# Kernel optimization log

Hardware: AMD Instinct MI355X
Metric: run time of the kernel (lower is better)

The kernel has to match this reference:

```python
import jax, jax.numpy as jnp
import numpy as np

B, V, E, L, D = 4, 64, 1024, 1024, 256  # batch, vertices, edges/graph, seq_len, d_model
DEG = E // V


def setup_inputs() -> dict:
    key = jax.random.key(0)
    k0, k1, k2, k3, k4, k5 = jax.random.split(key, 6)
    # fixed 16-regular graph, edges sorted by (src, dst) so that nonzero()
    # extraction order of the dense adjacency equals a gather at (src, dst)
    src = np.repeat(np.arange(V), DEG)
    dst = (src + 1 + np.tile(np.arange(DEG), V)) % V
    order = np.lexsort((dst, src))
    src, dst = src[order], dst[order]
    edge_index = jnp.asarray(np.stack([np.tile(src, B), np.tile(dst, B)]), dtype=jnp.int32)
    hidden_states = jax.random.normal(k0, (B * V, L, D), dtype=jnp.float32)
    edge_weight = jax.random.uniform(k1, (B * E,), dtype=jnp.float32, minval=0.1, maxval=1.0)
    s = 0.02
    Wq = jax.random.normal(k2, (D, D), dtype=jnp.float32) * s
    bq = jax.random.normal(k3, (D,), dtype=jnp.float32) * s
    Wk = jax.random.normal(k4, (D, D), dtype=jnp.float32) * s
    bk = jax.random.normal(k5, (D,), dtype=jnp.float32) * s
    attn_skip = jnp.float32(0.5)
    return {"hidden_states": hidden_states, "edge_index": edge_index, "edge_weight": edge_weight,
            "Wq": Wq, "bq": bq, "Wk": Wk, "bk": bk, "attn_skip": attn_skip}


def reference(hidden_states, edge_index, edge_weight, Wq, bq, Wk, bk, attn_skip):
    # broadcast static edge list / weights across time, as the torch repeat does
    ei = jnp.broadcast_to(edge_index[:, :, None], (2, B * E, L))
    ew = jnp.broadcast_to(edge_weight[:, None], (B * E, L))
    hs = hidden_states.reshape(B, V, L, D)
    Q = hs @ Wq.T + bq  # nn.Linear: x W^T + b
    K = hs @ Wk.T + bk
    att = jnp.einsum('bvld,bwld->bvwl', Q, K) / jnp.sqrt(jnp.float32(D))
    bidx = jnp.repeat(jnp.arange(B), E)
    src, dst = edge_index[0], edge_index[1]
    # to_dense_adj: scatter-add edge weights -> (B, V, V, L)
    adj = jnp.zeros((B, V, V, L), att.dtype).at[bidx, src, dst, :].add(ew)
    mask = jnp.where(adj > 0, 0.0, -jnp.inf)
    att = jax.nn.softmax(att + mask, axis=2)  # softmax over destination vertices w
    adj_new = attn_skip * adj + (1.0 - attn_skip) * att
    # dense_to_sparse: nonzeros in (graph=b*L+l, row, col) row-major order.
    # Edges are sorted by (src,dst), so this is a gather; torch flat order is (b, l, e):
    g = adj_new[bidx, src, dst, :]  # (B*E, L) ordered (b, e, l)
    flat = g.reshape(B, E, L).transpose(0, 2, 1).reshape(-1)  # order (b, l, e)
    # replicate the original .view(B, E, L).transpose(1, 2).reshape(B*E, L)
    ew_out = flat.reshape(B, E, L).transpose(0, 2, 1).reshape(B * E, L)
    return ei, ew_out
```

## Files before the change

### kernel.cpp

```cpp
#include <hip/hip_runtime.h>
#include <cstdint>
#include <cstddef>

constexpr int Bv = 4;
constexpr int Ev = 1024;
constexpr int Lv = 1024;
constexpr int BE = Bv * Ev;
constexpr size_t EI_PLANE = (size_t)BE * Lv;

constexpr int STRB = 264;

typedef __bf16 bf16x8 __attribute__((ext_vector_type(8)));
typedef __bf16 bf16x4 __attribute__((ext_vector_type(4)));
typedef __bf16 bf16x2 __attribute__((ext_vector_type(2)));
typedef float  f32x4  __attribute__((ext_vector_type(4)));

static __device__ __forceinline__ unsigned int pack_bf2(float lo, float hi) {
    union { bf16x2 h; unsigned int u; } c;
    c.h[0] = (__bf16)lo; c.h[1] = (__bf16)hi;
    return c.u;
}

__global__ __launch_bounds__(256) void precompute_kernel(
    const float* __restrict__ Wq, const float* __restrict__ Wk,
    const float* __restrict__ bq, __bf16* __restrict__ Mb, float* __restrict__ rv)
{
    const int blk = blockIdx.x;
    const int tid = threadIdx.x;
    if (blk < 256) {
        __shared__ float qs[256 * 17];
        __shared__ float ks[256 * 17];
        const int i16 = (blk >> 4) * 16;
        const int j16 = (blk & 15) * 16;
        const int c  = tid & 15;
        const int r0 = tid >> 4;
        #pragma unroll
        for (int it = 0; it < 16; ++it) {
            const int r = it * 16 + r0;
            qs[r * 17 + c] = Wq[r * 256 + i16 + c];
            ks[r * 17 + c] = Wk[r * 256 + j16 + c];
        }
        __syncthreads();
        const int dd = tid >> 4;
        const int tt = tid & 15;
        float a0 = 0.f, a1 = 0.f, a2 = 0.f, a3 = 0.f;
        for (int r = 0; r < 256; r += 4) {
            a0 = fmaf(qs[(r + 0) * 17 + dd], ks[(r + 0) * 17 + tt], a0);
            a1 = fmaf(qs[(r + 1) * 17 + dd], ks[(r + 1) * 17 + tt], a1);
            a2 = fmaf(qs[(r + 2) * 17 + dd], ks[(r + 2) * 17 + tt], a2);
            a3 = fmaf(qs[(r + 3) * 17 + dd], ks[(r + 3) * 17 + tt], a3);
        }
        const float m = ((a0 + a1) + (a2 + a3)) * 0.0625f;
        const int d = i16 + dd, t = j16 + tt;
        const int f    = (d >> 5) * 16 + (t >> 4);
        const int lane = ((d >> 3) & 3) * 16 + (t & 15);
        const int jj   = d & 7;
        Mb[((size_t)f * 64 + lane) * 8 + jj] = (__bf16)m;
    } else {
        __shared__ float bqs[256];
        bqs[tid] = bq[tid];
        __syncthreads();
        float a0 = 0.f, a1 = 0.f;
        for (int i = 0; i < 256; i += 2) {
            a0 = fmaf(bqs[i + 0], Wk[(i + 0) * 256 + tid], a0);
            a1 = fmaf(bqs[i + 1], Wk[(i + 1) * 256 + tid], a1);
        }
        rv[tid] = (a0 + a1) * 0.0625f;
    }
}

template <bool USE_WS>
__global__ __launch_bounds__(256) void edge_main(
    const float* __restrict__ hs, const int* __restrict__ eidx,
    const float* __restrict__ ew, const float* __restrict__ skipp,
    const __bf16* __restrict__ Mb, const float* __restrict__ rv,
    float* __restrict__ probs_or_out)
{
    __shared__ __bf16 hs_s[64 * STRB];
    float* S0 = (float*)hs_s;

    const int bl = blockIdx.x;
    const int b  = bl >> 10;
    const int l  = bl & 1023;
    const int tid  = threadIdx.x;
    const int w    = tid >> 6;
    const int lane = tid & 63;
    const int l15  = lane & 15;
    const int quad = lane >> 4;
    const int vgrp  = w >> 1;
    const int thalf = w & 1;

    {
        const float* base = hs + ((size_t)b * 64 * 1024 + (size_t)l) * 256;
        const int half = lane >> 5;
        const int c8   = (lane & 31) * 8;
        #pragma unroll
        for (int k = 0; k < 8; ++k) {
            const int v = k * 8 + w * 2 + half;
            const float* p = base + (size_t)v * (1024 * 256) + c8;
            float4 va = *(const float4*)p;
            float4 vb = *(const float4*)(p + 4);
            bf16x8 h;
            h[0] = (__bf16)va.x; h[1] = (__bf16)va.y;
            h[2] = (__bf16)va.z; h[3] = (__bf16)va.w;
            h[4] = (__bf16)vb.x; h[5] = (__bf16)vb.y;
            h[6] = (__bf16)vb.z; h[7] = (__bf16)vb.w;
            *(bf16x8*)(&hs_s[v * STRB + c8]) = h;
        }
    }
    __syncthreads();

    f32x4 s_acc[2][2];
    #pragma unroll
    for (int mi = 0; mi < 2; ++mi)
        #pragma unroll
        for (int sl = 0; sl < 2; ++sl) {
            s_acc[mi][sl][0] = 0.f; s_acc[mi][sl][1] = 0.f;
            s_acc[mi][sl][2] = 0.f; s_acc[mi][sl][3] = 0.f;
        }

    const int vt0 = vgrp * 2;

    #pragma unroll 1
    for (int pp = 0; pp < 4; ++pp) {
        const int p = thalf * 4 + pp;
        f32x4 acc[2][2];
        #pragma unroll
        for (int tt = 0; tt < 2; ++tt) {
            const f32x4 rb = *(const f32x4*)(rv + (2 * p + tt) * 16 + quad * 4);
            acc[tt][0] = rb;
            acc[tt][1] = rb;
        }
        #pragma unroll
        for (int kt = 0; kt < 8; ++kt) {
            const bf16x8 mfr0 = *(const bf16x8*)(Mb +
                ((size_t)((kt * 16 + 2 * p + 0) * 64 + lane)) * 8);
            const bf16x8 mfr1 = *(const bf16x8*)(Mb +
                ((size_t)((kt * 16 + 2 * p + 1) * 64 + lane)) * 8);
            #pragma unroll
            for (int mi = 0; mi < 2; ++mi) {
                const bf16x8 hfr = *(const bf16x8*)(
                    &hs_s[((vt0 + mi) * 16 + l15) * STRB + kt * 32 + quad * 8]);
                acc[0][mi] = __builtin_amdgcn_mfma_f32_16x16x32_bf16(
                    mfr0, hfr, acc[0][mi], 0, 0, 0);
                acc[1][mi] = __builtin_amdgcn_mfma_f32_16x16x32_bf16(
                    mfr1, hfr, acc[1][mi], 0, 0, 0);
            }
        }
        #pragma unroll
        for (int mi = 0; mi < 2; ++mi) {
            const int m = vt0 + mi;
            unsigned int Ar = pack_bf2(acc[0][mi][0], acc[0][mi][1]);
            unsigned int Br = pack_bf2(acc[0][mi][2], acc[0][mi][3]);
            unsigned int Cr = pack_bf2(acc[1][mi][0], acc[1][mi][1]);
            unsigned int Dr = pack_bf2(acc[1][mi][2], acc[1][mi][3]);
            asm("v_permlane32_swap_b32 %0, %1" : "+v"(Ar), "+v"(Cr));
            asm("v_permlane16_swap_b32 %0, %1" : "+v"(Ar), "+v"(Cr));
            asm("v_permlane32_swap_b32 %0, %1" : "+v"(Br), "+v"(Dr));
            asm("v_permlane16_swap_b32 %0, %1" : "+v"(Br), "+v"(Dr));
            union { uint4 u; bf16x8 h; } fr;
            fr.u = make_uint4(Ar, Br, Cr, Dr);
            const bf16x8 brow0 = *(const bf16x8*)(
                &hs_s[(m * 16 + l15) * STRB + p * 32 + quad * 8]);
            const bf16x8 brow1 = *(const bf16x8*)(
                &hs_s[(((m + 1) & 3) * 16 + l15) * STRB + p * 32 + quad * 8]);
            s_acc[mi][0] = __builtin_amdgcn_mfma_f32_16x16x32_bf16(
                fr.h, brow0, s_acc[mi][0], 0, 0, 0);
            s_acc[mi][1] = __builtin_amdgcn_mfma_f32_16x16x32_bf16(
                fr.h, brow1, s_acc[mi][1], 0, 0, 0);
        }
    }
    __syncthreads();

    if (!thalf) {
        #pragma unroll
        for (int mi = 0; mi < 2; ++mi)
            #pragma unroll
            for (int sl = 0; sl < 2; ++sl)
                #pragma unroll
                for (int r = 0; r < 4; ++r)
                    S0[((vt0 + mi) * 16 + quad * 4 + r) * 36 + sl * 16 + l15] =
                        s_acc[mi][sl][r];
    }
    __syncthreads();
    if (thalf) {
        #pragma unroll
        for (int mi = 0; mi < 2; ++mi)
            #pragma unroll
            for (int sl = 0; sl < 2; ++sl)
                #pragma unroll
                for (int r = 0; r < 4; ++r)
                    S0[((vt0 + mi) * 16 + quad * 4 + r) * 36 + sl * 16 + l15] +=
                        s_acc[mi][sl][r];
    }
    __syncthreads();

    const int e0  = tid * 4;
    const int be0 = b * Ev + e0;
    int srcs[4], dsts[4];
    #pragma unroll
    for (int j = 0; j < 4; ++j) {
        srcs[j] = eidx[be0 + j];
        dsts[j] = eidx[BE + be0 + j];
    }
    float lg[4];
    #pragma unroll
    for (int j = 0; j < 4; ++j) {
        const int slot = ((dsts[j] >> 4) - (srcs[j] >> 4)) & 3;
        lg[j] = S0[srcs[j] * 36 + slot * 16 + (dsts[j] & 15)];
    }

    float mx = fmaxf(fmaxf(lg[0], lg[1]), fmaxf(lg[2], lg[3]));
    mx = fmaxf(mx, __shfl_xor(mx, 1));
    mx = fmaxf(mx, __shfl_xor(mx, 2));
    float ex[4], sm = 0.f;
    #pragma unroll
    for (int j = 0; j < 4; ++j) { ex[j] = __expf(lg[j] - mx); sm += ex[j]; }
    sm += __shfl_xor(sm, 1);
    sm += __shfl_xor(sm, 2);
    const float inv = 1.0f / sm;

    if (USE_WS) {
        float4 o = make_float4(ex[0] * inv, ex[1] * inv, ex[2] * inv, ex[3] * inv);
        *(float4*)(probs_or_out + (size_t)bl * 1024 + e0) = o;
    } else {
        const float skip = skipp[0];
        const float om = 1.0f - skip;
        #pragma unroll
        for (int j = 0; j < 4; ++j) {
            float g = fmaf(skip, ew[be0 + j], om * (ex[j] * inv));
            probs_or_out[(size_t)(be0 + j) * Lv + l] = g;
        }
    }
}

__global__ __launch_bounds__(256) void output_kernel(
    const float* __restrict__ probs, const int* __restrict__ eidx,
    const float* __restrict__ ew, const float* __restrict__ skipp,
    float* __restrict__ out)
{
    __shared__ float tile[64 * 68];
    const int lt = blockIdx.x;
    const int et = blockIdx.y;
    const int b  = blockIdx.z;
    const int t  = threadIdx.x;
    const int tr = t >> 4;
    const int tc = t & 15;

    #pragma unroll
    for (int q = 0; q < 4; ++q) {
        const int lloc = q * 16 + tr;
        float4 v = *(const float4*)(probs +
            ((size_t)(b * 1024 + lt * 64 + lloc)) * 1024 + et * 64 + tc * 4);
        *(float4*)(&tile[lloc * 68 + tc * 4]) = v;
    }
    __syncthreads();

    const float skip = skipp[0];
    const float om = 1.0f - skip;
    float* out_ei0 = out;
    float* out_ei1 = out + EI_PLANE;
    float* out_ew  = out + 2 * EI_PLANE;

    #pragma unroll
    for (int q = 0; q < 4; ++q) {
        const int eloc = q * 16 + tr;
        const int be = b * Ev + et * 64 + eloc;
        const float w  = ew[be];
        const float sv = (float)eidx[be];
        const float dv = (float)eidx[BE + be];
        const int lloc0 = tc * 4;
        float4 o;
        o.x = fmaf(skip, w, om * tile[(lloc0 + 0) * 68 + eloc]);
        o.y = fmaf(skip, w, om * tile[(lloc0 + 1) * 68 + eloc]);
        o.z = fmaf(skip, w, om * tile[(lloc0 + 2) * 68 + eloc]);
        o.w = fmaf(skip, w, om * tile[(lloc0 + 3) * 68 + eloc]);
        const size_t off = (size_t)be * Lv + lt * 64 + lloc0;
        *(float4*)(out_ew  + off) = o;
        *(float4*)(out_ei0 + off) = make_float4(sv, sv, sv, sv);
        *(float4*)(out_ei1 + off) = make_float4(dv, dv, dv, dv);
    }
}

__global__ __launch_bounds__(256) void ei_kernel(
    const int* __restrict__ eidx, float* __restrict__ out)
{
    const int blk = blockIdx.x;
    const int c = blk >> 12;
    const int j = blk & 4095;
    const float v = (float)eidx[c * BE + j];
    float4 o = make_float4(v, v, v, v);
    *(float4*)(out + (size_t)blk * 1024 + threadIdx.x * 4) = o;
}

extern "C" void kernel_launch(void* const* d_in, const int* in_sizes, int n_in,
                              void* d_out, int out_size, void* d_ws, size_t ws_size,
                              hipStream_t stream)
{
    const float* hs   = (const float*)d_in[0];
    const int*   eidx = (const int*)d_in[1];
    const float* ew   = (const float*)d_in[2];
    const float* Wq   = (const float*)d_in[3];
    const float* bq   = (const float*)d_in[4];
    const float* Wk   = (const float*)d_in[5];
    const float* skip = (const float*)d_in[7];

    char* wsb = (char*)d_ws;
    __bf16* Mb   = (__bf16*)wsb;
    float*  rv   = (float*)(wsb + 131072);
    float*  probs = (float*)(wsb + 132096);
    const size_t need = 132096 + (size_t)Bv * Lv * Ev * sizeof(float);

    precompute_kernel<<<dim3(257), dim3(256), 0, stream>>>(Wq, Wk, bq, Mb, rv);

    if (ws_size >= need) {
        edge_main<true><<<dim3(Bv * Lv), dim3(256), 0, stream>>>(
            hs, eidx, ew, skip, Mb, rv, probs);
        output_kernel<<<dim3(16, 16, 4), dim3(256), 0, stream>>>(
            probs, eidx, ew, skip, (float*)d_out);
    } else {
        float* out_ew = (float*)d_out + 2 * EI_PLANE;
        edge_main<false><<<dim3(Bv * Lv), dim3(256), 0, stream>>>(
            hs, eidx, ew, skip, Mb, rv, out_ew);
        ei_kernel<<<dim3(2 * BE), dim3(256), 0, stream>>>(eidx, (float*)d_out);
    }
}
```

Measured before the change: 445.0 us.

## Process eight time steps per block with double-buffered register prefetch of hidden states

```diff
diff --git a/kernel.cpp b/kernel.cpp
--- a/kernel.cpp
+++ b/kernel.cpp
@@ -9,6 +9,7 @@
 constexpr size_t EI_PLANE = (size_t)BE * Lv;
 
 constexpr int STRB = 264;
+constexpr int NL = 8;
 
 typedef __bf16 bf16x8 __attribute__((ext_vector_type(8)));
 typedef __bf16 bf16x4 __attribute__((ext_vector_type(4)));
@@ -70,18 +71,17 @@
 }
 
 template <bool USE_WS>
-__global__ __launch_bounds__(256) void edge_main(
+__global__ __launch_bounds__(256, 2) void edge_main(
     const float* __restrict__ hs, const int* __restrict__ eidx,
     const float* __restrict__ ew, const float* __restrict__ skipp,
     const __bf16* __restrict__ Mb, const float* __restrict__ rv,
     float* __restrict__ probs_or_out)
 {
-    __shared__ __bf16 hs_s[64 * STRB];
-    float* S0 = (float*)hs_s;
-
-    const int bl = blockIdx.x;
-    const int b  = bl >> 10;
-    const int l  = bl & 1023;
+    __shared__ __bf16 hs2_s[2][64 * STRB];
+
+    const int blk = blockIdx.x;
+    const int b   = blk >> 7;
+    const int l0  = (blk & 127) * NL;
     const int tid  = threadIdx.x;
     const int w    = tid >> 6;
     const int lane = tid & 63;
@@ -89,11 +89,25 @@
     const int quad = lane >> 4;
     const int vgrp  = w >> 1;
     const int thalf = w & 1;
+    const int vt0   = vgrp * 2;
+    const int half  = lane >> 5;
+    const int c8    = (lane & 31) * 8;
+
+    const float* hb = hs + (size_t)b * 65536 * 256;
+
+    const int e0  = tid * 4;
+    const int be0 = b * Ev + e0;
+    int soff[4];
+    #pragma unroll
+    for (int j = 0; j < 4; ++j) {
+        const int src = eidx[be0 + j];
+        const int dst = eidx[BE + be0 + j];
+        const int slot = ((dst >> 4) - (src >> 4)) & 3;
+        soff[j] = src * 36 + slot * 16 + (dst & 15);
+    }
 
     {
-        const float* base = hs + ((size_t)b * 64 * 1024 + (size_t)l) * 256;
-        const int half = lane >> 5;
-        const int c8   = (lane & 31) * 8;
+        const float* base = hb + (size_t)l0 * 256;
         #pragma unroll
         for (int k = 0; k < 8; ++k) {
             const int v = k * 8 + w * 2 + half;
@@ -105,132 +119,154 @@
             h[2] = (__bf16)va.z; h[3] = (__bf16)va.w;
             h[4] = (__bf16)vb.x; h[5] = (__bf16)vb.y;
             h[6] = (__bf16)vb.z; h[7] = (__bf16)vb.w;
-            *(bf16x8*)(&hs_s[v * STRB + c8]) = h;
+            *(bf16x8*)(&hs2_s[0][v * STRB + c8]) = h;
         }
     }
     __syncthreads();
 
-    f32x4 s_acc[2][2];
-    #pragma unroll
-    for (int mi = 0; mi < 2; ++mi)
-        #pragma unroll
-        for (int sl = 0; sl < 2; ++sl) {
-            s_acc[mi][sl][0] = 0.f; s_acc[mi][sl][1] = 0.f;
-            s_acc[mi][sl][2] = 0.f; s_acc[mi][sl][3] = 0.f;
-        }
-
-    const int vt0 = vgrp * 2;
-
+    int cur = 0;
     #pragma unroll 1
-    for (int pp = 0; pp < 4; ++pp) {
-        const int p = thalf * 4 + pp;
-        f32x4 acc[2][2];
-        #pragma unroll
-        for (int tt = 0; tt < 2; ++tt) {
-            const f32x4 rb = *(const f32x4*)(rv + (2 * p + tt) * 16 + quad * 4);
-            acc[tt][0] = rb;
-            acc[tt][1] = rb;
-        }
-        #pragma unroll
-        for (int kt = 0; kt < 8; ++kt) {
-            const bf16x8 mfr0 = *(const bf16x8*)(Mb +
-                ((size_t)((kt * 16 + 2 * p + 0) * 64 + lane)) * 8);
-            const bf16x8 mfr1 = *(const bf16x8*)(Mb +
-                ((size_t)((kt * 16 + 2 * p + 1) * 64 + lane)) * 8);
+    for (int i = 0; i < NL; ++i) {
+        const int l = l0 + i;
+        __bf16* bufc = &hs2_s[cur][0];
+        float*  S0   = (float*)bufc;
+
+        const int lnext = (i + 1 < NL) ? (l + 1) : l;
+        const float* basen = hb + (size_t)lnext * 256;
+        float4 pf[16];
+        #pragma unroll
+        for (int k = 0; k < 8; ++k) {
+            const float* p = basen + (size_t)(k * 8 + w * 2 + half) * (1024 * 256) + c8;
+            pf[2 * k]     = *(const float4*)p;
+            pf[2 * k + 1] = *(const float4*)(p + 4);
+        }
+
+        f32x4 s_acc[2][2];
+        #pragma unroll
+        for (int mi = 0; mi < 2; ++mi)
+            #pragma unroll
+            for (int sl = 0; sl < 2; ++sl) {
+                s_acc[mi][sl][0] = 0.f; s_acc[mi][sl][1] = 0.f;
+                s_acc[mi][sl][2] = 0.f; s_acc[mi][sl][3] = 0.f;
+            }
+
+        #pragma unroll 1
+        for (int pp = 0; pp < 4; ++pp) {
+            const int p = thalf * 4 + pp;
+            f32x4 acc[2][2];
+            #pragma unroll
+            for (int tt = 0; tt < 2; ++tt) {
+                const f32x4 rb = *(const f32x4*)(rv + (2 * p + tt) * 16 + quad * 4);
+                acc[tt][0] = rb;
+                acc[tt][1] = rb;
+            }
+            #pragma unroll
+            for (int kt = 0; kt < 8; ++kt) {
+                const bf16x8 mfr0 = *(const bf16x8*)(Mb +
+                    ((size_t)((kt * 16 + 2 * p + 0) * 64 + lane)) * 8);
+                const bf16x8 mfr1 = *(const bf16x8*)(Mb +
+                    ((size_t)((kt * 16 + 2 * p + 1) * 64 + lane)) * 8);
+                #pragma unroll
+                for (int mi = 0; mi < 2; ++mi) {
+                    const bf16x8 hfr = *(const bf16x8*)(
+                        &bufc[((vt0 + mi) * 16 + l15) * STRB + kt * 32 + quad * 8]);
+                    acc[0][mi] = __builtin_amdgcn_mfma_f32_16x16x32_bf16(
+                        mfr0, hfr, acc[0][mi], 0, 0, 0);
+                    acc[1][mi] = __builtin_amdgcn_mfma_f32_16x16x32_bf16(
+                        mfr1, hfr, acc[1][mi], 0, 0, 0);
+                }
+            }
             #pragma unroll
             for (int mi = 0; mi < 2; ++mi) {
-                const bf16x8 hfr = *(const bf16x8*)(
-                    &hs_s[((vt0 + mi) * 16 + l15) * STRB + kt * 32 + quad * 8]);
-                acc[0][mi] = __builtin_amdgcn_mfma_f32_16x16x32_bf16(
-                    mfr0, hfr, acc[0][mi], 0, 0, 0);
-                acc[1][mi] = __builtin_amdgcn_mfma_f32_16x16x32_bf16(
-                    mfr1, hfr, acc[1][mi], 0, 0, 0);
-            }
-        }
-        #pragma unroll
-        for (int mi = 0; mi < 2; ++mi) {
-            const int m = vt0 + mi;
-            unsigned int Ar = pack_bf2(acc[0][mi][0], acc[0][mi][1]);
-            unsigned int Br = pack_bf2(acc[0][mi][2], acc[0][mi][3]);
-            unsigned int Cr = pack_bf2(acc[1][mi][0], acc[1][mi][1]);
-            unsigned int Dr = pack_bf2(acc[1][mi][2], acc[1][mi][3]);
-            asm("v_permlane32_swap_b32 %0, %1" : "+v"(Ar), "+v"(Cr));
-            asm("v_permlane16_swap_b32 %0, %1" : "+v"(Ar), "+v"(Cr));
-            asm("v_permlane32_swap_b32 %0, %1" : "+v"(Br), "+v"(Dr));
-            asm("v_permlane16_swap_b32 %0, %1" : "+v"(Br), "+v"(Dr));
-            union { uint4 u; bf16x8 h; } fr;
-            fr.u = make_uint4(Ar, Br, Cr, Dr);
-            const bf16x8 brow0 = *(const bf16x8*)(
-                &hs_s[(m * 16 + l15) * STRB + p * 32 + quad * 8]);
-            const bf16x8 brow1 = *(const bf16x8*)(
-                &hs_s[(((m + 1) & 3) * 16 + l15) * STRB + p * 32 + quad * 8]);
-            s_acc[mi][0] = __builtin_amdgcn_mfma_f32_16x16x32_bf16(
-                fr.h, brow0, s_acc[mi][0], 0, 0, 0);
-            s_acc[mi][1] = __builtin_amdgcn_mfma_f32_16x16x32_bf16(
-                fr.h, brow1, s_acc[mi][1], 0, 0, 0);
-        }
-    }
-    __syncthreads();
-
-    if (!thalf) {
-        #pragma unroll
-        for (int mi = 0; mi < 2; ++mi)
-            #pragma unroll
-            for (int sl = 0; sl < 2; ++sl)
+                const int m = vt0 + mi;
+                unsigned int Ar = pack_bf2(acc[0][mi][0], acc[0][mi][1]);
+                unsigned int Br = pack_bf2(acc[0][mi][2], acc[0][mi][3]);
+                unsigned int Cr = pack_bf2(acc[1][mi][0], acc[1][mi][1]);
+                unsigned int Dr = pack_bf2(acc[1][mi][2], acc[1][mi][3]);
+                asm("v_permlane32_swap_b32 %0, %1" : "+v"(Ar), "+v"(Cr));
+                asm("v_permlane16_swap_b32 %0, %1" : "+v"(Ar), "+v"(Cr));
+                asm("v_permlane32_swap_b32 %0, %1" : "+v"(Br), "+v"(Dr));
+                asm("v_permlane16_swap_b32 %0, %1" : "+v"(Br), "+v"(Dr));
+                union { uint4 u; bf16x8 h; } fr;
+                fr.u = make_uint4(Ar, Br, Cr, Dr);
+                const bf16x8 brow0 = *(const bf16x8*)(
+                    &bufc[(m * 16 + l15) * STRB + p * 32 + quad * 8]);
+                const bf16x8 brow1 = *(const bf16x8*)(
+                    &bufc[(((m + 1) & 3) * 16 + l15) * STRB + p * 32 + quad * 8]);
+                s_acc[mi][0] = __builtin_amdgcn_mfma_f32_16x16x32_bf16(
+                    fr.h, brow0, s_acc[mi][0], 0, 0, 0);
+                s_acc[mi][1] = __builtin_amdgcn_mfma_f32_16x16x32_bf16(
+                    fr.h, brow1, s_acc[mi][1], 0, 0, 0);
+            }
+        }
+        __syncthreads();
+
+        if (!thalf) {
+            #pragma unroll
+            for (int mi = 0; mi < 2; ++mi)
                 #pragma unroll
-                for (int r = 0; r < 4; ++r)
-                    S0[((vt0 + mi) * 16 + quad * 4 + r) * 36 + sl * 16 + l15] =
-                        s_acc[mi][sl][r];
-    }
-    __syncthreads();
-    if (thalf) {
-        #pragma unroll
-        for (int mi = 0; mi < 2; ++mi)
-            #pragma unroll
-            for (int sl = 0; sl < 2; ++sl)
+                for (int sl = 0; sl < 2; ++sl)
+                    #pragma unroll
+                    for (int r = 0; r < 4; ++r)
+                        S0[((vt0 + mi) * 16 + quad * 4 + r) * 36 + sl * 16 + l15] =
+                            s_acc[mi][sl][r];
+        }
+        __syncthreads();
+        if (thalf) {
+            #pragma unroll
+            for (int mi = 0; mi < 2; ++mi)
                 #pragma unroll
-                for (int r = 0; r < 4; ++r)
-                    S0[((vt0 + mi) * 16 + quad * 4 + r) * 36 + sl * 16 + l15] +=
-                        s_acc[mi][sl][r];
-    }
-    __syncthreads();
-
-    const int e0  = tid * 4;
-    const int be0 = b * Ev + e0;
-    int srcs[4], dsts[4];
-    #pragma unroll
-    for (int j = 0; j < 4; ++j) {
-        srcs[j] = eidx[be0 + j];
-        dsts[j] = eidx[BE + be0 + j];
-    }
-    float lg[4];
-    #pragma unroll
-    for (int j = 0; j < 4; ++j) {
-        const int slot = ((dsts[j] >> 4) - (srcs[j] >> 4)) & 3;
-        lg[j] = S0[srcs[j] * 36 + slot * 16 + (dsts[j] & 15)];
-    }
-
-    float mx = fmaxf(fmaxf(lg[0], lg[1]), fmaxf(lg[2], lg[3]));
-    mx = fmaxf(mx, __shfl_xor(mx, 1));
-    mx = fmaxf(mx, __shfl_xor(mx, 2));
-    float ex[4], sm = 0.f;
-    #pragma unroll
-    for (int j = 0; j < 4; ++j) { ex[j] = __expf(lg[j] - mx); sm += ex[j]; }
-    sm += __shfl_xor(sm, 1);
-    sm += __shfl_xor(sm, 2);
-    const float inv = 1.0f / sm;
-
-    if (USE_WS) {
-        float4 o = make_float4(ex[0] * inv, ex[1] * inv, ex[2] * inv, ex[3] * inv);
-        *(float4*)(probs_or_out + (size_t)bl * 1024 + e0) = o;
-    } else {
-        const float skip = skipp[0];
-        const float om = 1.0f - skip;
-        #pragma unroll
-        for (int j = 0; j < 4; ++j) {
-            float g = fmaf(skip, ew[be0 + j], om * (ex[j] * inv));
-            probs_or_out[(size_t)(be0 + j) * Lv + l] = g;
-        }
+                for (int sl = 0; sl < 2; ++sl)
+                    #pragma unroll
+                    for (int r = 0; r < 4; ++r)
+                        S0[((vt0 + mi) * 16 + quad * 4 + r) * 36 + sl * 16 + l15] +=
+                            s_acc[mi][sl][r];
+        }
+        __syncthreads();
+
+        float lg[4];
+        #pragma unroll
+        for (int j = 0; j < 4; ++j)
+            lg[j] = S0[soff[j]];
+
+        float mx = fmaxf(fmaxf(lg[0], lg[1]), fmaxf(lg[2], lg[3]));
+        mx = fmaxf(mx, __shfl_xor(mx, 1));
+        mx = fmaxf(mx, __shfl_xor(mx, 2));
+        float ex[4], sm = 0.f;
+        #pragma unroll
+        for (int j = 0; j < 4; ++j) { ex[j] = __expf(lg[j] - mx); sm += ex[j]; }
+        sm += __shfl_xor(sm, 1);
+        sm += __shfl_xor(sm, 2);
+        const float inv = 1.0f / sm;
+
+        if (USE_WS) {
+            float4 o = make_float4(ex[0] * inv, ex[1] * inv, ex[2] * inv, ex[3] * inv);
+            *(float4*)(probs_or_out + ((size_t)(b * 1024 + l)) * 1024 + e0) = o;
+        } else {
+            const float skip = skipp[0];
+            const float om = 1.0f - skip;
+            #pragma unroll
+            for (int j = 0; j < 4; ++j) {
+                float g = fmaf(skip, ew[be0 + j], om * (ex[j] * inv));
+                probs_or_out[(size_t)(be0 + j) * Lv + l] = g;
+            }
+        }
+
+        {
+            __bf16* bufn = &hs2_s[cur ^ 1][0];
+            #pragma unroll
+            for (int k = 0; k < 8; ++k) {
+                const int v = k * 8 + w * 2 + half;
+                bf16x8 h;
+                h[0] = (__bf16)pf[2 * k].x;     h[1] = (__bf16)pf[2 * k].y;
+                h[2] = (__bf16)pf[2 * k].z;     h[3] = (__bf16)pf[2 * k].w;
+                h[4] = (__bf16)pf[2 * k + 1].x; h[5] = (__bf16)pf[2 * k + 1].y;
+                h[6] = (__bf16)pf[2 * k + 1].z; h[7] = (__bf16)pf[2 * k + 1].w;
+                *(bf16x8*)(&bufn[v * STRB + c8]) = h;
+            }
+        }
+        __syncthreads();
+        cur ^= 1;
     }
 }
 
@@ -314,13 +350,13 @@
     precompute_kernel<<<dim3(257), dim3(256), 0, stream>>>(Wq, Wk, bq, Mb, rv);
 
     if (ws_size >= need) {
-        edge_main<true><<<dim3(Bv * Lv), dim3(256), 0, stream>>>(
+        edge_main<true><<<dim3(Bv * Lv / NL), dim3(256), 0, stream>>>(
             hs, eidx, ew, skip, Mb, rv, probs);
         output_kernel<<<dim3(16, 16, 4), dim3(256), 0, stream>>>(
             probs, eidx, ew, skip, (float*)d_out);
     } else {
         float* out_ew = (float*)d_out + 2 * EI_PLANE;
-        edge_main<false><<<dim3(Bv * Lv), dim3(256), 0, stream>>>(
+        edge_main<false><<<dim3(Bv * Lv / NL), dim3(256), 0, stream>>>(
             hs, eidx, ew, skip, Mb, rv, out_ew);
         ei_kernel<<<dim3(2 * BE), dim3(256), 0, stream>>>(eidx, (float*)d_out);
     }
```

Measured after the change: 476.9 us. +7.2%, slower.

## Give each wave one vertex tile across all p-chunks, dropping split-K reduction

Applied to the files above, without the earlier changes.

```diff
diff --git a/kernel.cpp b/kernel.cpp
--- a/kernel.cpp
+++ b/kernel.cpp
@@ -70,7 +70,7 @@
 }
 
 template <bool USE_WS>
-__global__ __launch_bounds__(256) void edge_main(
+__global__ __launch_bounds__(256, 4) void edge_main(
     const float* __restrict__ hs, const int* __restrict__ eidx,
     const float* __restrict__ ew, const float* __restrict__ skipp,
     const __bf16* __restrict__ Mb, const float* __restrict__ rv,
@@ -87,8 +87,18 @@
     const int lane = tid & 63;
     const int l15  = lane & 15;
     const int quad = lane >> 4;
-    const int vgrp  = w >> 1;
-    const int thalf = w & 1;
+    const int nt1  = (w + 1) & 3;
+
+    const int e0  = tid * 4;
+    const int be0 = b * Ev + e0;
+    int soff[4];
+    #pragma unroll
+    for (int j = 0; j < 4; ++j) {
+        const int src = eidx[be0 + j];
+        const int dst = eidx[BE + be0 + j];
+        const int slot = ((dst >> 4) - (src >> 4)) & 3;
+        soff[j] = src * 36 + slot * 16 + (dst & 15);
+    }
 
     {
         const float* base = hs + ((size_t)b * 64 * 1024 + (size_t)l) * 256;
@@ -110,105 +120,70 @@
     }
     __syncthreads();
 
-    f32x4 s_acc[2][2];
-    #pragma unroll
-    for (int mi = 0; mi < 2; ++mi)
+    bf16x8 hfrK[8];
+    #pragma unroll
+    for (int kt = 0; kt < 8; ++kt)
+        hfrK[kt] = *(const bf16x8*)(&hs_s[(w * 16 + l15) * STRB + kt * 32 + quad * 8]);
+
+    f32x4 s_acc0, s_acc1;
+    s_acc0[0] = 0.f; s_acc0[1] = 0.f; s_acc0[2] = 0.f; s_acc0[3] = 0.f;
+    s_acc1 = s_acc0;
+
+    #pragma unroll 1
+    for (int p = 0; p < 8; ++p) {
+        f32x4 acc0 = *(const f32x4*)(rv + (2 * p + 0) * 16 + quad * 4);
+        f32x4 acc1 = *(const f32x4*)(rv + (2 * p + 1) * 16 + quad * 4);
         #pragma unroll
-        for (int sl = 0; sl < 2; ++sl) {
-            s_acc[mi][sl][0] = 0.f; s_acc[mi][sl][1] = 0.f;
-            s_acc[mi][sl][2] = 0.f; s_acc[mi][sl][3] = 0.f;
-        }
-
-    const int vt0 = vgrp * 2;
-
-    #pragma unroll 1
-    for (int pp = 0; pp < 4; ++pp) {
-        const int p = thalf * 4 + pp;
-        f32x4 acc[2][2];
-        #pragma unroll
-        for (int tt = 0; tt < 2; ++tt) {
-            const f32x4 rb = *(const f32x4*)(rv + (2 * p + tt) * 16 + quad * 4);
-            acc[tt][0] = rb;
-            acc[tt][1] = rb;
-        }
-        #pragma unroll
-        for (int kt = 0; kt < 8; ++kt) {
-            const bf16x8 mfr0 = *(const bf16x8*)(Mb +
-                ((size_t)((kt * 16 + 2 * p + 0) * 64 + lane)) * 8);
-            const bf16x8 mfr1 = *(const bf16x8*)(Mb +
-                ((size_t)((kt * 16 + 2 * p + 1) * 64 + lane)) * 8);
+        for (int kh = 0; kh < 2; ++kh) {
+            bf16x8 m0[4], m1[4];
             #pragma unroll
-            for (int mi = 0; mi < 2; ++mi) {
-                const bf16x8 hfr = *(const bf16x8*)(
-                    &hs_s[((vt0 + mi) * 16 + l15) * STRB + kt * 32 + quad * 8]);
-                acc[0][mi] = __builtin_amdgcn_mfma_f32_16x16x32_bf16(
-                    mfr0, hfr, acc[0][mi], 0, 0, 0);
-                acc[1][mi] = __builtin_amdgcn_mfma_f32_16x16x32_bf16(
-                    mfr1, hfr, acc[1][mi], 0, 0, 0);
+            for (int k2 = 0; k2 < 4; ++k2) {
+                const int kt = kh * 4 + k2;
+                m0[k2] = *(const bf16x8*)(Mb +
+                    ((size_t)((kt * 16 + 2 * p + 0) * 64 + lane)) * 8);
+                m1[k2] = *(const bf16x8*)(Mb +
+                    ((size_t)((kt * 16 + 2 * p + 1) * 64 + lane)) * 8);
             }
-        }
-        #pragma unroll
-        for (int mi = 0; mi < 2; ++mi) {
-            const int m = vt0 + mi;
-            unsigned int Ar = pack_bf2(acc[0][mi][0], acc[0][mi][1]);
-            unsigned int Br = pack_bf2(acc[0][mi][2], acc[0][mi][3]);
-            unsigned int Cr = pack_bf2(acc[1][mi][0], acc[1][mi][1]);
-            unsigned int Dr = pack_bf2(acc[1][mi][2], acc[1][mi][3]);
-            asm("v_permlane32_swap_b32 %0, %1" : "+v"(Ar), "+v"(Cr));
-            asm("v_permlane16_swap_b32 %0, %1" : "+v"(Ar), "+v"(Cr));
-            asm("v_permlane32_swap_b32 %0, %1" : "+v"(Br), "+v"(Dr));
-            asm("v_permlane16_swap_b32 %0, %1" : "+v"(Br), "+v"(Dr));
-            union { uint4 u; bf16x8 h; } fr;
-            fr.u = make_uint4(Ar, Br, Cr, Dr);
-            const bf16x8 brow0 = *(const bf16x8*)(
-                &hs_s[(m * 16 + l15) * STRB + p * 32 + quad * 8]);
-            const bf16x8 brow1 = *(const bf16x8*)(
-                &hs_s[(((m + 1) & 3) * 16 + l15) * STRB + p * 32 + quad * 8]);
-            s_acc[mi][0] = __builtin_amdgcn_mfma_f32_16x16x32_bf16(
-                fr.h, brow0, s_acc[mi][0], 0, 0, 0);
-            s_acc[mi][1] = __builtin_amdgcn_mfma_f32_16x16x32_bf16(
-                fr.h, brow1, s_acc[mi][1], 0, 0, 0);
-        }
+            #pragma unroll
+            for (int k2 = 0; k2 < 4; ++k2) {
+                const int kt = kh * 4 + k2;
+                acc0 = __builtin_amdgcn_mfma_f32_16x16x32_bf16(
+                    m0[k2], hfrK[kt], acc0, 0, 0, 0);
+                acc1 = __builtin_amdgcn_mfma_f32_16x16x32_bf16(
+                    m1[k2], hfrK[kt], acc1, 0, 0, 0);
+            }
+        }
+        unsigned int Ar = pack_bf2(acc0[0], acc0[1]);
+        unsigned int Br = pack_bf2(acc0[2], acc0[3]);
+        unsigned int Cr = pack_bf2(acc1[0], acc1[1]);
+        unsigned int Dr = pack_bf2(acc1[2], acc1[3]);
+        asm("v_permlane32_swap_b32 %0, %1" : "+v"(Ar), "+v"(Cr));
+        asm("v_permlane16_swap_b32 %0, %1" : "+v"(Ar), "+v"(Cr));
+        asm("v_permlane32_swap_b32 %0, %1" : "+v"(Br), "+v"(Dr));
+        asm("v_permlane16_swap_b32 %0, %1" : "+v"(Br), "+v"(Dr));
+        union { uint4 u; bf16x8 h; } fr;
+        fr.u = make_uint4(Ar, Br, Cr, Dr);
+
+        const bf16x8 brow0 = *(const bf16x8*)(
+            &hs_s[(w * 16 + l15) * STRB + p * 32 + quad * 8]);
+        const bf16x8 brow1 = *(const bf16x8*)(
+            &hs_s[(nt1 * 16 + l15) * STRB + p * 32 + quad * 8]);
+        s_acc0 = __builtin_amdgcn_mfma_f32_16x16x32_bf16(fr.h, brow0, s_acc0, 0, 0, 0);
+        s_acc1 = __builtin_amdgcn_mfma_f32_16x16x32_bf16(fr.h, brow1, s_acc1, 0, 0, 0);
     }
     __syncthreads();
 
-    if (!thalf) {
-        #pragma unroll
-        for (int mi = 0; mi < 2; ++mi)
-            #pragma unroll
-            for (int sl = 0; sl < 2; ++sl)
-                #pragma unroll
-                for (int r = 0; r < 4; ++r)
-                    S0[((vt0 + mi) * 16 + quad * 4 + r) * 36 + sl * 16 + l15] =
-                        s_acc[mi][sl][r];
+    #pragma unroll
+    for (int r = 0; r < 4; ++r) {
+        S0[(w * 16 + quad * 4 + r) * 36 +  0 + l15] = s_acc0[r];
+        S0[(w * 16 + quad * 4 + r) * 36 + 16 + l15] = s_acc1[r];
     }
     __syncthreads();
-    if (thalf) {
-        #pragma unroll
-        for (int mi = 0; mi < 2; ++mi)
-            #pragma unroll
-            for (int sl = 0; sl < 2; ++sl)
-                #pragma unroll
-                for (int r = 0; r < 4; ++r)
-                    S0[((vt0 + mi) * 16 + quad * 4 + r) * 36 + sl * 16 + l15] +=
-                        s_acc[mi][sl][r];
-    }
-    __syncthreads();
-
-    const int e0  = tid * 4;
-    const int be0 = b * Ev + e0;
-    int srcs[4], dsts[4];
-    #pragma unroll
-    for (int j = 0; j < 4; ++j) {
-        srcs[j] = eidx[be0 + j];
-        dsts[j] = eidx[BE + be0 + j];
-    }
+
     float lg[4];
     #pragma unroll
-    for (int j = 0; j < 4; ++j) {
-        const int slot = ((dsts[j] >> 4) - (srcs[j] >> 4)) & 3;
-        lg[j] = S0[srcs[j] * 36 + slot * 16 + (dsts[j] & 15)];
-    }
+    for (int j = 0; j < 4; ++j)
+        lg[j] = S0[soff[j]];
 
     float mx = fmaxf(fmaxf(lg[0], lg[1]), fmaxf(lg[2], lg[3]));
     mx = fmaxf(mx, __shfl_xor(mx, 1));
```

New measurement: 451.7 us. About the same (+1.5%).
